# Optimization experiments

Measured on AMD Instinct MI355X. Metric: run time of the kernel, lower is better.

## Reference

```python
import jax, jax.numpy as jnp
import numpy as np

RHO = 1.0
MU = 1e-05
DT = 1.0 / 32
DX = 1.0 / 255
DY = 1.0 / 255


def _residuals(x, std):
    # x: [B, 3, H, W]; torch does x *= std (pure version here)
    x = x * std
    u = x[:, 0]  # [B, H, W]
    v = x[:, 1]
    p = x[:, 2]
    r = jnp.roll

    dudt = (r(u, -1, 0) - r(u, 1, 0)) / DT
    dvdt = (r(v, -1, 0) - r(v, 1, 0)) / DT
    dudx = (r(u, -1, 1) - r(u, 1, 1)) / (2 * DX)
    dudy = (r(u, -1, 2) - r(u, 1, 2)) / (2 * DY)
    dvdx = (r(v, -1, 1) - r(v, 1, 1)) / (2 * DX)
    dvdy = (r(v, -1, 2) - r(v, 1, 2)) / (2 * DY)
    dpdx = (r(p, -1, 1) - r(p, 1, 1)) / (2 * DX)
    dpdy = (r(p, -1, 2) - r(p, 1, 2)) / (2 * DY)
    d2udx2 = (r(u, -1, 1) - 2 * u + r(u, 1, 1)) / DX ** 2
    d2udy2 = (r(u, -1, 2) - 2 * u + r(u, 1, 2)) / DY ** 2
    d2vdx2 = (r(v, -1, 1) - 2 * v + r(v, 1, 1)) / DX ** 2
    d2vdy2 = (r(v, -1, 2) - 2 * v + r(v, 1, 2)) / DY ** 2

    t = lambda a: a[1:-1, 1:-1, 1:-1]  # trim periodic-wrap halo
    u, v = t(u), t(v)
    r0 = jnp.abs(t(dudx) + t(dvdy))
    r1 = jnp.abs(RHO * (t(dudt) + u * t(dudx) + v * t(dudy)) + t(dpdx)
                 - MU * (t(d2udx2) + t(d2udy2)))
    r2 = jnp.abs(RHO * (t(dvdt) + u * t(dvdx) + v * t(dvdy)) + t(dpdy)
                 - MU * (t(d2vdx2) + t(d2vdy2)))
    return r0, r1, r2


def setup_inputs() -> dict:
    key = jax.random.key(0)
    k1, k2, k3 = jax.random.split(key, 3)
    B, C, H, W = 64, 3, 512, 512
    x = jax.random.normal(k1, (B, C, H, W), dtype=jnp.float32)
    y = jax.random.normal(k2, (B, C, H, W), dtype=jnp.float32)
    std = jax.random.uniform(k3, (), dtype=jnp.float32)
    return {"x": x, "y": y, "std": std}


def reference(x, y, std):
    r0_y, r1_y, r2_y = _residuals(y, std)
    r0_x, r1_x, r2_x = _residuals(x, std)
    d0 = jnp.mean((r0_y - r0_x) ** 2)
    d1 = jnp.mean((r1_y - r1_x) ** 2)
    d2 = jnp.mean((r2_y - r2_x) ** 2)
    return 0.001 * (d0 + d1 + d2)
```

## Files before the change

### kernel.cpp

```cpp
#include <hip/hip_runtime.h>


constexpr int Wd   = 512;
constexpr int CSTR = 512 * 512;
constexpr int BSTR = 3 * 512 * 512;

__device__ __forceinline__ float4 ld4(const float* p) {
    return *reinterpret_cast<const float4*>(p);
}
__device__ __forceinline__ float4 scale4(float4 a, float s) {
    return make_float4(a.x * s, a.y * s, a.z * s, a.w * s);
}

__device__ __forceinline__ void residuals(
    const float* __restrict__ T, int c, int jt, float s, float sdx,
    float4 un, float4 vn, float4 uc, float4 vc, float4 um, float4 vm,
    float4 uu, float4 ud, float4 vu, float4 vd,
    float4 pu, float4 pd, float4 pc,
    float r0[4], float r1[4], float r2[4])
{
    float u_l = __shfl_up(uc.w, 1);
    float v_l = __shfl_up(vc.w, 1);
    float p_l = __shfl_up(pc.w, 1);
    float u_r = __shfl_down(uc.x, 1);
    float v_r = __shfl_down(vc.x, 1);
    float p_r = __shfl_down(pc.x, 1);
    if (jt == 64) {
        u_l = T[c - 1] * s;
        v_l = T[c + CSTR - 1] * s;
        p_l = T[c + 2 * CSTR - 1];
    }
    if (jt == 63) {
        u_r = T[c + 4] * s;
        v_r = T[c + CSTR + 4] * s;
        p_r = T[c + 2 * CSTR + 4];
    }

    const float ucA[4] = {uc.x, uc.y, uc.z, uc.w};
    const float vcA[4] = {vc.x, vc.y, vc.z, vc.w};
    const float umA[4] = {um.x, um.y, um.z, um.w};
    const float vmA[4] = {vm.x, vm.y, vm.z, vm.w};
    const float unA[4] = {un.x, un.y, un.z, un.w};
    const float vnA[4] = {vn.x, vn.y, vn.z, vn.w};
    const float ul[4]  = {u_l, uc.x, uc.y, uc.z};
    const float ur[4]  = {uc.y, uc.z, uc.w, u_r};
    const float vl[4]  = {v_l, vc.x, vc.y, vc.z};
    const float vr[4]  = {vc.y, vc.z, vc.w, v_r};
    const float pl[4]  = {p_l, pc.x, pc.y, pc.z};
    const float pr[4]  = {pc.y, pc.z, pc.w, p_r};
    const float uuA[4] = {uu.x, uu.y, uu.z, uu.w};
    const float udA[4] = {ud.x, ud.y, ud.z, ud.w};
    const float vuA[4] = {vu.x, vu.y, vu.z, vu.w};
    const float vdA[4] = {vd.x, vd.y, vd.z, vd.w};
    const float puA[4] = {pu.x, pu.y, pu.z, pu.w};
    const float pdA[4] = {pd.x, pd.y, pd.z, pd.w};

    #pragma unroll
    for (int k = 0; k < 4; ++k) {
        const float dudx = (uuA[k] - udA[k]) * 127.5f;
        const float dvdx = (vuA[k] - vdA[k]) * 127.5f;
        const float dpdx = (puA[k] - pdA[k]) * sdx;
        const float dudy = (ur[k] - ul[k]) * 127.5f;
        const float dvdy = (vr[k] - vl[k]) * 127.5f;
        const float dpdy = (pr[k] - pl[k]) * sdx;
        const float lapu = (uuA[k] + udA[k] + ur[k] + ul[k]) * 0.65025f
                         - 2.601f * ucA[k];
        const float lapv = (vuA[k] + vdA[k] + vr[k] + vl[k]) * 0.65025f
                         - 2.601f * vcA[k];
        r0[k] = fabsf(dudx + dvdy);
        r1[k] = fabsf((unA[k] - umA[k]) * 32.0f + ucA[k] * dudx + vcA[k] * dudy
                      + dpdx - lapu);
        r2[k] = fabsf((vnA[k] - vmA[k]) * 32.0f + ucA[k] * dvdx + vcA[k] * dvdy
                      + dpdy - lapv);
    }
}

__global__ __launch_bounds__(512)
void ns_loss_kernel(const float* __restrict__ X, const float* __restrict__ Y,
                    const float* __restrict__ stdp, double* __restrict__ acc)
{
    __shared__ float4 lds[2][3][4][128];
    __shared__ float sm[3][8];

    const float s   = *stdp;
    const float sdx = s * 127.5f;

    const int orig = blockIdx.x;
    const int wg   = (orig & 7) * 96 + (orig >> 3);
    const int z    = wg / 128;
    const int band = wg % 128;

    const int tid = threadIdx.x;
    const int io  = tid >> 7;
    const int jt  = tid & 127;
    const int j0  = jt << 2;
    const int irow = 1 + band * 4 + io;
    const int i    = min(irow, 511);
    const bool vrow = (irow <= 510);
    const int bs = 1 + 11 * z;
    const int nsteps = min(11, 62 - 11 * z);

    int c = bs * BSTR + i * Wd + j0;
    const int cup = (i < 511) ? Wd : 0;

    float4 xum = scale4(ld4(X + c - BSTR), s);
    float4 xuc = scale4(ld4(X + c), s);
    float4 xvm = scale4(ld4(X + c - BSTR + CSTR), s);
    float4 xvc = scale4(ld4(X + c + CSTR), s);
    float4 yum = scale4(ld4(Y + c - BSTR), s);
    float4 yuc = scale4(ld4(Y + c), s);
    float4 yvm = scale4(ld4(Y + c - BSTR + CSTR), s);
    float4 yvc = scale4(ld4(Y + c + CSTR), s);

    float s0 = 0.0f, s1 = 0.0f, s2 = 0.0f;

    float4 xuN = make_float4(0,0,0,0), xvN = xuN, xpN = xuN;
    float4 yuN = xuN, yvN = xuN, ypN = xuN;

    for (int it = 0; it < nsteps; ++it) {
        const float4 xun = scale4(ld4(X + c + BSTR), s);
        const float4 xvn = scale4(ld4(X + c + BSTR + CSTR), s);
        const float4 yun = scale4(ld4(Y + c + BSTR), s);
        const float4 yvn = scale4(ld4(Y + c + BSTR + CSTR), s);
        const float4 xpc = ld4(X + c + 2 * CSTR);
        const float4 ypc = ld4(Y + c + 2 * CSTR);
        if (io == 0) {
            xuN = scale4(ld4(X + c - Wd), s);
            xvN = scale4(ld4(X + c + CSTR - Wd), s);
            xpN = ld4(X + c + 2 * CSTR - Wd);
            yuN = scale4(ld4(Y + c - Wd), s);
            yvN = scale4(ld4(Y + c + CSTR - Wd), s);
            ypN = ld4(Y + c + 2 * CSTR - Wd);
        } else if (io == 3) {
            xuN = scale4(ld4(X + c + cup), s);
            xvN = scale4(ld4(X + c + CSTR + cup), s);
            xpN = ld4(X + c + 2 * CSTR + cup);
            yuN = scale4(ld4(Y + c + cup), s);
            yvN = scale4(ld4(Y + c + CSTR + cup), s);
            ypN = ld4(Y + c + 2 * CSTR + cup);
        }

        lds[0][0][io][jt] = xuc;  lds[0][1][io][jt] = xvc;  lds[0][2][io][jt] = xpc;
        lds[1][0][io][jt] = yuc;  lds[1][1][io][jt] = yvc;  lds[1][2][io][jt] = ypc;
        __syncthreads();

        float4 xud, xvd, xpd, yud, yvd, ypd;
        float4 xuu, xvu, xpu, yuu, yvu, ypu;
        if (io > 0) {
            xud = lds[0][0][io-1][jt]; xvd = lds[0][1][io-1][jt]; xpd = lds[0][2][io-1][jt];
            yud = lds[1][0][io-1][jt]; yvd = lds[1][1][io-1][jt]; ypd = lds[1][2][io-1][jt];
        } else { xud = xuN; xvd = xvN; xpd = xpN; yud = yuN; yvd = yvN; ypd = ypN; }
        if (io < 3) {
            xuu = lds[0][0][io+1][jt]; xvu = lds[0][1][io+1][jt]; xpu = lds[0][2][io+1][jt];
            yuu = lds[1][0][io+1][jt]; yvu = lds[1][1][io+1][jt]; ypu = lds[1][2][io+1][jt];
        } else { xuu = xuN; xvu = xvN; xpu = xpN; yuu = yuN; yvu = yvN; ypu = ypN; }

        float r0x[4], r1x[4], r2x[4], r0y[4], r1y[4], r2y[4];
        residuals(X, c, jt, s, sdx, xun, xvn, xuc, xvc, xum, xvm,
                  xuu, xud, xvu, xvd, xpu, xpd, xpc, r0x, r1x, r2x);
        residuals(Y, c, jt, s, sdx, yun, yvn, yuc, yvc, yum, yvm,
                  yuu, yud, yvu, yvd, ypu, ypd, ypc, r0y, r1y, r2y);

        #pragma unroll
        for (int k = 0; k < 4; ++k) {
            float e0 = r0y[k] - r0x[k];
            float e1 = r1y[k] - r1x[k];
            float e2 = r2y[k] - r2x[k];
            const bool dead = (!vrow) || (k == 0 && j0 == 0)
                                      || (k == 3 && j0 == 508);
            if (dead) { e0 = 0.0f; e1 = 0.0f; e2 = 0.0f; }
            s0 += e0 * e0; s1 += e1 * e1; s2 += e2 * e2;
        }

        __syncthreads();

        xum = xuc; xuc = xun; xvm = xvc; xvc = xvn;
        yum = yuc; yuc = yun; yvm = yvc; yvc = yvn;
        c += BSTR;
    }

    for (int o = 32; o > 0; o >>= 1) {
        s0 += __shfl_down(s0, o);
        s1 += __shfl_down(s1, o);
        s2 += __shfl_down(s2, o);
    }
    const int wid = tid >> 6, lane = tid & 63;
    if (lane == 0) { sm[0][wid] = s0; sm[1][wid] = s1; sm[2][wid] = s2; }
    __syncthreads();
    if (tid == 0) {
        double t0 = 0, t1 = 0, t2 = 0;
        #pragma unroll
        for (int w = 0; w < 8; ++w) {
            t0 += (double)sm[0][w]; t1 += (double)sm[1][w]; t2 += (double)sm[2][w];
        }
        atomicAdd(&acc[0], t0);
        atomicAdd(&acc[1], t1);
        atomicAdd(&acc[2], t2);
    }
}

__global__ void ns_finalize_kernel(const double* __restrict__ acc,
                                   float* __restrict__ out)
{
    if (threadIdx.x == 0) {
        const double N = 62.0 * 510.0 * 510.0;
        out[0] = (float)(1.0e-3 * (acc[0] + acc[1] + acc[2]) / N);
    }
}

extern "C" void kernel_launch(void* const* d_in, const int* in_sizes, int n_in,
                              void* d_out, int out_size, void* d_ws, size_t ws_size,
                              hipStream_t stream) {
    const float* X    = (const float*)d_in[0];
    const float* Y    = (const float*)d_in[1];
    const float* stdp = (const float*)d_in[2];
    float* out  = (float*)d_out;
    double* acc = (double*)d_ws;

    hipMemsetAsync(acc, 0, 3 * sizeof(double), stream);

    dim3 block(512);
    dim3 grid(128 * 6);
    ns_loss_kernel<<<grid, block, 0, stream>>>(X, Y, stdp, acc);
    ns_finalize_kernel<<<1, 64, 0, stream>>>(acc, out);
}
```

Measured before the change: 141.8 us.

## Prefetch next batch slice in registers and source wave-edge halos from LDS

Loads for the next batch step (u/v next, p current, edge-row halos) are issued right after the LDS barrier, so global latency overlaps the current step's stencil math. Barriers become raw s_barrier calls with explicit lgkmcnt waits. The global reloads of left/right neighbours at wave boundaries are replaced by scalar LDS reads from a float-indexed layout. The grid shrinks from 768 to 512 blocks, with 15-16 batch steps per block instead of 11. This raises register pressure and lowers parallelism in exchange for latency hiding.

```diff
diff --git a/kernel.cpp b/kernel.cpp
--- a/kernel.cpp
+++ b/kernel.cpp
@@ -12,60 +12,75 @@
     return make_float4(a.x * s, a.y * s, a.z * s, a.w * s);
 }
 
-__device__ __forceinline__ void residuals(
-    const float* __restrict__ T, int c, int jt, float s, float sdx,
-    float4 un, float4 vn, float4 uc, float4 vc, float4 um, float4 vm,
-    float4 uu, float4 ud, float4 vu, float4 vd,
-    float4 pu, float4 pd, float4 pc,
+__device__ __forceinline__ void plane_resid(
+    const float (&L)[3][4][512],
+    int io, int jt, int j0,
+    float4 eu, float4 ev, float4 ep,
+    float4 mu, float4 cu, float4 nus,
+    float4 mv, float4 cv, float4 nvs,
+    float4 cp, float sdx,
     float r0[4], float r1[4], float r2[4])
 {
-    float u_l = __shfl_up(uc.w, 1);
-    float v_l = __shfl_up(vc.w, 1);
-    float p_l = __shfl_up(pc.w, 1);
-    float u_r = __shfl_down(uc.x, 1);
-    float v_r = __shfl_down(vc.x, 1);
-    float p_r = __shfl_down(pc.x, 1);
-    if (jt == 64) {
-        u_l = T[c - 1] * s;
-        v_l = T[c + CSTR - 1] * s;
-        p_l = T[c + 2 * CSTR - 1];
-    }
-    if (jt == 63) {
-        u_r = T[c + 4] * s;
-        v_r = T[c + CSTR + 4] * s;
-        p_r = T[c + 2 * CSTR + 4];
-    }
-
-    const float ucA[4] = {uc.x, uc.y, uc.z, uc.w};
-    const float vcA[4] = {vc.x, vc.y, vc.z, vc.w};
-    const float umA[4] = {um.x, um.y, um.z, um.w};
-    const float vmA[4] = {vm.x, vm.y, vm.z, vm.w};
-    const float unA[4] = {un.x, un.y, un.z, un.w};
-    const float vnA[4] = {vn.x, vn.y, vn.z, vn.w};
-    const float ul[4]  = {u_l, uc.x, uc.y, uc.z};
-    const float ur[4]  = {uc.y, uc.z, uc.w, u_r};
-    const float vl[4]  = {v_l, vc.x, vc.y, vc.z};
-    const float vr[4]  = {vc.y, vc.z, vc.w, v_r};
-    const float pl[4]  = {p_l, pc.x, pc.y, pc.z};
-    const float pr[4]  = {pc.y, pc.z, pc.w, p_r};
-    const float uuA[4] = {uu.x, uu.y, uu.z, uu.w};
-    const float udA[4] = {ud.x, ud.y, ud.z, ud.w};
-    const float vuA[4] = {vu.x, vu.y, vu.z, vu.w};
-    const float vdA[4] = {vd.x, vd.y, vd.z, vd.w};
-    const float puA[4] = {pu.x, pu.y, pu.z, pu.w};
-    const float pdA[4] = {pd.x, pd.y, pd.z, pd.w};
+    float4 uxm, vxm, pxm, uxp, vxp, pxp;
+    if (io == 0) { uxm = eu; vxm = ev; pxm = ep; }
+    else {
+        uxm = ld4(&L[0][io - 1][j0]);
+        vxm = ld4(&L[1][io - 1][j0]);
+        pxm = ld4(&L[2][io - 1][j0]);
+    }
+    if (io == 3) { uxp = eu; vxp = ev; pxp = ep; }
+    else {
+        uxp = ld4(&L[0][io + 1][j0]);
+        vxp = ld4(&L[1][io + 1][j0]);
+        pxp = ld4(&L[2][io + 1][j0]);
+    }
+
+    float u_l = __shfl_up(cu.w, 1);
+    float v_l = __shfl_up(cv.w, 1);
+    float p_l = __shfl_up(cp.w, 1);
+    float u_r = __shfl_down(cu.x, 1);
+    float v_r = __shfl_down(cv.x, 1);
+    float p_r = __shfl_down(cp.x, 1);
+    const int lane = jt & 63;
+    if (lane == 0) {
+        const int jm = (j0 == 0) ? 0 : (j0 - 1);
+        u_l = L[0][io][jm]; v_l = L[1][io][jm]; p_l = L[2][io][jm];
+    }
+    if (lane == 63) {
+        const int jp = (j0 >= 508) ? 511 : (j0 + 4);
+        u_r = L[0][io][jp]; v_r = L[1][io][jp]; p_r = L[2][io][jp];
+    }
+
+    const float ucA[4] = {cu.x, cu.y, cu.z, cu.w};
+    const float vcA[4] = {cv.x, cv.y, cv.z, cv.w};
+    const float umA[4] = {mu.x, mu.y, mu.z, mu.w};
+    const float vmA[4] = {mv.x, mv.y, mv.z, mv.w};
+    const float unA[4] = {nus.x, nus.y, nus.z, nus.w};
+    const float vnA[4] = {nvs.x, nvs.y, nvs.z, nvs.w};
+    const float ul[4]  = {u_l, cu.x, cu.y, cu.z};
+    const float ur[4]  = {cu.y, cu.z, cu.w, u_r};
+    const float vl[4]  = {v_l, cv.x, cv.y, cv.z};
+    const float vr[4]  = {cv.y, cv.z, cv.w, v_r};
+    const float pl[4]  = {p_l, cp.x, cp.y, cp.z};
+    const float pr[4]  = {cp.y, cp.z, cp.w, p_r};
+    const float uxpA[4] = {uxp.x, uxp.y, uxp.z, uxp.w};
+    const float uxmA[4] = {uxm.x, uxm.y, uxm.z, uxm.w};
+    const float vxpA[4] = {vxp.x, vxp.y, vxp.z, vxp.w};
+    const float vxmA[4] = {vxm.x, vxm.y, vxm.z, vxm.w};
+    const float pxpA[4] = {pxp.x, pxp.y, pxp.z, pxp.w};
+    const float pxmA[4] = {pxm.x, pxm.y, pxm.z, pxm.w};
 
     #pragma unroll
     for (int k = 0; k < 4; ++k) {
-        const float dudx = (uuA[k] - udA[k]) * 127.5f;
-        const float dvdx = (vuA[k] - vdA[k]) * 127.5f;
-        const float dpdx = (puA[k] - pdA[k]) * sdx;
+        const float dudx = (uxpA[k] - uxmA[k]) * 127.5f;
+        const float dvdx = (vxpA[k] - vxmA[k]) * 127.5f;
+        const float dpdx = (pxpA[k] - pxmA[k]) * sdx;
         const float dudy = (ur[k] - ul[k]) * 127.5f;
         const float dvdy = (vr[k] - vl[k]) * 127.5f;
         const float dpdy = (pr[k] - pl[k]) * sdx;
-        const float lapu = (uuA[k] + udA[k] + ur[k] + ul[k]) * 0.65025f
+        const float lapu = (uxpA[k] + uxmA[k] + ur[k] + ul[k]) * 0.65025f
                          - 2.601f * ucA[k];
-        const float lapv = (vuA[k] + vdA[k] + vr[k] + vl[k]) * 0.65025f
+        const float lapv = (vxpA[k] + vxmA[k] + vr[k] + vl[k]) * 0.65025f
                          - 2.601f * vcA[k];
         r0[k] = fabsf(dudx + dvdy);
         r1[k] = fabsf((unA[k] - umA[k]) * 32.0f + ucA[k] * dudx + vcA[k] * dudy
@@ -79,87 +94,95 @@
 void ns_loss_kernel(const float* __restrict__ X, const float* __restrict__ Y,
                     const float* __restrict__ stdp, double* __restrict__ acc)
 {
-    __shared__ float4 lds[2][3][4][128];
-    __shared__ float sm[3][8];
+    __shared__ float lds[2][3][4][512];
+    __shared__ float smr[3][8];
 
     const float s   = *stdp;
     const float sdx = s * 127.5f;
 
     const int orig = blockIdx.x;
-    const int wg   = (orig & 7) * 96 + (orig >> 3);
-    const int z    = wg / 128;
-    const int band = wg % 128;
+    const int wg   = (orig & 7) * 64 + (orig >> 3);
+    const int z    = wg >> 7;
+    const int band = wg & 127;
 
     const int tid = threadIdx.x;
+    const int jt  = tid & 127;
     const int io  = tid >> 7;
-    const int jt  = tid & 127;
     const int j0  = jt << 2;
     const int irow = 1 + band * 4 + io;
     const int i    = min(irow, 511);
     const bool vrow = (irow <= 510);
-    const int bs = 1 + 11 * z;
-    const int nsteps = min(11, 62 - 11 * z);
+    const int bs = 1 + 15 * z + (z == 3 ? 1 : 0);
+    const int nsteps = (z < 2) ? 15 : 16;
 
     int c = bs * BSTR + i * Wd + j0;
-    const int cup = (i < 511) ? Wd : 0;
-
-    float4 xum = scale4(ld4(X + c - BSTR), s);
-    float4 xuc = scale4(ld4(X + c), s);
-    float4 xvm = scale4(ld4(X + c - BSTR + CSTR), s);
-    float4 xvc = scale4(ld4(X + c + CSTR), s);
-    float4 yum = scale4(ld4(Y + c - BSTR), s);
-    float4 yuc = scale4(ld4(Y + c), s);
-    float4 yvm = scale4(ld4(Y + c - BSTR + CSTR), s);
-    float4 yvc = scale4(ld4(Y + c + CSTR), s);
+    const int cup  = (i < 511) ? Wd : 0;
+    const int eoff = (io == 0) ? -Wd : cup;
+    const bool isedge = (io == 0) || (io == 3);
+
+    float4 xmu = scale4(ld4(X + c - BSTR), s);
+    float4 xcu = scale4(ld4(X + c), s);
+    float4 xmv = scale4(ld4(X + c - BSTR + CSTR), s);
+    float4 xcv = scale4(ld4(X + c + CSTR), s);
+    float4 ymu = scale4(ld4(Y + c - BSTR), s);
+    float4 ycu = scale4(ld4(Y + c), s);
+    float4 ymv = scale4(ld4(Y + c - BSTR + CSTR), s);
+    float4 ycv = scale4(ld4(Y + c + CSTR), s);
+    float4 xnu = ld4(X + c + BSTR);
+    float4 xnv = ld4(X + c + BSTR + CSTR);
+    float4 xcp = ld4(X + c + 2 * CSTR);
+    float4 ynu = ld4(Y + c + BSTR);
+    float4 ynv = ld4(Y + c + BSTR + CSTR);
+    float4 ycp = ld4(Y + c + 2 * CSTR);
+    float4 xeu = make_float4(0,0,0,0), xev = xeu, xep = xeu;
+    float4 yeu = xeu, yev = xeu, yep = xeu;
+    if (isedge) {
+        xeu = scale4(ld4(X + c + eoff), s);
+        xev = scale4(ld4(X + c + CSTR + eoff), s);
+        xep = ld4(X + c + 2 * CSTR + eoff);
+        yeu = scale4(ld4(Y + c + eoff), s);
+        yev = scale4(ld4(Y + c + CSTR + eoff), s);
+        yep = ld4(Y + c + 2 * CSTR + eoff);
+    }
 
     float s0 = 0.0f, s1 = 0.0f, s2 = 0.0f;
 
-    float4 xuN = make_float4(0,0,0,0), xvN = xuN, xpN = xuN;
-    float4 yuN = xuN, yvN = xuN, ypN = xuN;
-
     for (int it = 0; it < nsteps; ++it) {
-        const float4 xun = scale4(ld4(X + c + BSTR), s);
-        const float4 xvn = scale4(ld4(X + c + BSTR + CSTR), s);
-        const float4 yun = scale4(ld4(Y + c + BSTR), s);
-        const float4 yvn = scale4(ld4(Y + c + BSTR + CSTR), s);
-        const float4 xpc = ld4(X + c + 2 * CSTR);
-        const float4 ypc = ld4(Y + c + 2 * CSTR);
-        if (io == 0) {
-            xuN = scale4(ld4(X + c - Wd), s);
-            xvN = scale4(ld4(X + c + CSTR - Wd), s);
-            xpN = ld4(X + c + 2 * CSTR - Wd);
-            yuN = scale4(ld4(Y + c - Wd), s);
-            yvN = scale4(ld4(Y + c + CSTR - Wd), s);
-            ypN = ld4(Y + c + 2 * CSTR - Wd);
-        } else if (io == 3) {
-            xuN = scale4(ld4(X + c + cup), s);
-            xvN = scale4(ld4(X + c + CSTR + cup), s);
-            xpN = ld4(X + c + 2 * CSTR + cup);
-            yuN = scale4(ld4(Y + c + cup), s);
-            yvN = scale4(ld4(Y + c + CSTR + cup), s);
-            ypN = ld4(Y + c + 2 * CSTR + cup);
+        const int cn = c + ((it + 1 < nsteps) ? BSTR : 0);
+
+        *(float4*)&lds[0][0][io][j0] = xcu;
+        *(float4*)&lds[0][1][io][j0] = xcv;
+        *(float4*)&lds[0][2][io][j0] = xcp;
+        *(float4*)&lds[1][0][io][j0] = ycu;
+        *(float4*)&lds[1][1][io][j0] = ycv;
+        *(float4*)&lds[1][2][io][j0] = ycp;
+        asm volatile("s_waitcnt lgkmcnt(0)" ::: "memory");
+        __builtin_amdgcn_s_barrier();
+
+        const float4 xnus = scale4(xnu, s), xnvs = scale4(xnv, s);
+        const float4 ynus = scale4(ynu, s), ynvs = scale4(ynv, s);
+        xnu = ld4(X + cn + BSTR);
+        xnv = ld4(X + cn + BSTR + CSTR);
+        ynu = ld4(Y + cn + BSTR);
+        ynv = ld4(Y + cn + BSTR + CSTR);
+        float4 xcp2 = ld4(X + cn + 2 * CSTR);
+        float4 ycp2 = ld4(Y + cn + 2 * CSTR);
+        float4 xeu2 = xeu, xev2 = xev, xep2 = xep;
+        float4 yeu2 = yeu, yev2 = yev, yep2 = yep;
+        if (isedge) {
+            xeu2 = scale4(ld4(X + cn + eoff), s);
+            xev2 = scale4(ld4(X + cn + CSTR + eoff), s);
+            xep2 = ld4(X + cn + 2 * CSTR + eoff);
+            yeu2 = scale4(ld4(Y + cn + eoff), s);
+            yev2 = scale4(ld4(Y + cn + CSTR + eoff), s);
+            yep2 = ld4(Y + cn + 2 * CSTR + eoff);
         }
 
-        lds[0][0][io][jt] = xuc;  lds[0][1][io][jt] = xvc;  lds[0][2][io][jt] = xpc;
-        lds[1][0][io][jt] = yuc;  lds[1][1][io][jt] = yvc;  lds[1][2][io][jt] = ypc;
-        __syncthreads();
-
-        float4 xud, xvd, xpd, yud, yvd, ypd;
-        float4 xuu, xvu, xpu, yuu, yvu, ypu;
-        if (io > 0) {
-            xud = lds[0][0][io-1][jt]; xvd = lds[0][1][io-1][jt]; xpd = lds[0][2][io-1][jt];
-            yud = lds[1][0][io-1][jt]; yvd = lds[1][1][io-1][jt]; ypd = lds[1][2][io-1][jt];
-        } else { xud = xuN; xvd = xvN; xpd = xpN; yud = yuN; yvd = yvN; ypd = ypN; }
-        if (io < 3) {
-            xuu = lds[0][0][io+1][jt]; xvu = lds[0][1][io+1][jt]; xpu = lds[0][2][io+1][jt];
-            yuu = lds[1][0][io+1][jt]; yvu = lds[1][1][io+1][jt]; ypu = lds[1][2][io+1][jt];
-        } else { xuu = xuN; xvu = xvN; xpu = xpN; yuu = yuN; yvu = yvN; ypu = ypN; }
-
         float r0x[4], r1x[4], r2x[4], r0y[4], r1y[4], r2y[4];
-        residuals(X, c, jt, s, sdx, xun, xvn, xuc, xvc, xum, xvm,
-                  xuu, xud, xvu, xvd, xpu, xpd, xpc, r0x, r1x, r2x);
-        residuals(Y, c, jt, s, sdx, yun, yvn, yuc, yvc, yum, yvm,
-                  yuu, yud, yvu, yvd, ypu, ypd, ypc, r0y, r1y, r2y);
+        plane_resid(lds[0], io, jt, j0, xeu, xev, xep,
+                    xmu, xcu, xnus, xmv, xcv, xnvs, xcp, sdx, r0x, r1x, r2x);
+        plane_resid(lds[1], io, jt, j0, yeu, yev, yep,
+                    ymu, ycu, ynus, ymv, ycv, ynvs, ycp, sdx, r0y, r1y, r2y);
 
         #pragma unroll
         for (int k = 0; k < 4; ++k) {
@@ -172,11 +195,14 @@
             s0 += e0 * e0; s1 += e1 * e1; s2 += e2 * e2;
         }
 
-        __syncthreads();
-
-        xum = xuc; xuc = xun; xvm = xvc; xvc = xvn;
-        yum = yuc; yuc = yun; yvm = yvc; yvc = yvn;
-        c += BSTR;
+        xmu = xcu; xcu = xnus; xmv = xcv; xcv = xnvs;
+        ymu = ycu; ycu = ynus; ymv = ycv; ycv = ynvs;
+        xcp = xcp2; ycp = ycp2;
+        xeu = xeu2; xev = xev2; xep = xep2;
+        yeu = yeu2; yev = yev2; yep = yep2;
+        asm volatile("s_waitcnt lgkmcnt(0)" ::: "memory");
+        __builtin_amdgcn_s_barrier();
+        c = cn;
     }
 
     for (int o = 32; o > 0; o >>= 1) {
@@ -185,13 +211,15 @@
         s2 += __shfl_down(s2, o);
     }
     const int wid = tid >> 6, lane = tid & 63;
-    if (lane == 0) { sm[0][wid] = s0; sm[1][wid] = s1; sm[2][wid] = s2; }
+    if (lane == 0) { smr[0][wid] = s0; smr[1][wid] = s1; smr[2][wid] = s2; }
     __syncthreads();
     if (tid == 0) {
         double t0 = 0, t1 = 0, t2 = 0;
         #pragma unroll
         for (int w = 0; w < 8; ++w) {
-            t0 += (double)sm[0][w]; t1 += (double)sm[1][w]; t2 += (double)sm[2][w];
+            t0 += (double)smr[0][w];
+            t1 += (double)smr[1][w];
+            t2 += (double)smr[2][w];
         }
         atomicAdd(&acc[0], t0);
         atomicAdd(&acc[1], t1);
@@ -220,7 +248,7 @@
     hipMemsetAsync(acc, 0, 3 * sizeof(double), stream);
 
     dim3 block(512);
-    dim3 grid(128 * 6);
+    dim3 grid(512);
     ns_loss_kernel<<<grid, block, 0, stream>>>(X, Y, stdp, acc);
     ns_finalize_kernel<<<1, 64, 0, stream>>>(acc, out);
 }
```

Result: faster. 124.3 us (-12.3%).
